# Kernel optimization log

Hardware: AMD Instinct MI355X
Metric: run time of the kernel (lower is better)

Reference implementation:

```python
import jax, jax.numpy as jnp
import numpy as np

B, S, H, I = 4, 2048, 4096, 11008

def setup_inputs() -> dict:
    key = jax.random.key(0)
    k0, k1, k2, k3 = jax.random.split(key, 4)
    scale = 0.02  # typical init scale for stability
    return {
        "x": jax.random.normal(k0, (B, S, H), dtype=jnp.float32),
        "w_gate": jax.random.normal(k1, (I, H), dtype=jnp.float32) * scale,
        "w_up": jax.random.normal(k2, (I, H), dtype=jnp.float32) * scale,
        "w_down": jax.random.normal(k3, (H, I), dtype=jnp.float32) * scale,
    }

def reference(x, w_gate, w_up, w_down):
    # gate = x @ w_gate^T, up = x @ w_up^T  (torch F.linear convention)
    gate = jnp.einsum("bsh,ih->bsi", x, w_gate)
    up = jnp.einsum("bsh,ih->bsi", x, w_up)
    inter = jax.nn.silu(gate) * up  # SwiGLU
    return jnp.einsum("bsi,hi->bsh", inter, w_down)
```

## Files before the change

kernel.cpp:

```cpp
#include <hip/hip_runtime.h>
#include <hip/hip_bf16.h>
#include <stdint.h>

static constexpr int Hd = 4096;
static constexpr int Id = 11008;
static constexpr int Md = 8192;

using short8 = __attribute__((ext_vector_type(8))) short;
using f32x4  = __attribute__((ext_vector_type(4))) float;

__device__ __forceinline__ unsigned short f2bf(float x) {
    union { float f; unsigned u; } v; v.f = x;
    unsigned r = v.u + 0x7FFF + ((v.u >> 16) & 1);
    return (unsigned short)(r >> 16);
}

typedef const __attribute__((address_space(1))) unsigned int* as1_u32p;
typedef __attribute__((address_space(3))) unsigned int* as3_u32p;

__device__ __forceinline__ void gload16(const unsigned short* g, unsigned short* l) {
    __builtin_amdgcn_global_load_lds((as1_u32p)(const void*)g, (as3_u32p)(void*)l, 16, 0, 0);
}

#define AOFF(r, c) ((((r) * 8) + ((c) ^ ((r) & 7))) * 8)

#define LGKM0() do { asm volatile("s_waitcnt lgkmcnt(0)" ::: "memory"); \
                     __builtin_amdgcn_sched_barrier(0); } while (0)
#define LGKMC8() do { asm volatile("s_waitcnt lgkmcnt(8)" ::: "memory"); } while (0)
#define VMCNT(n) do { asm volatile("s_waitcnt vmcnt(" #n ")" ::: "memory"); \
                      __builtin_amdgcn_sched_barrier(0); } while (0)
#define BARRIER() do { asm volatile("" ::: "memory"); __builtin_amdgcn_s_barrier(); \
                       asm volatile("" ::: "memory"); } while (0)

__global__ __launch_bounds__(256) void k_cvt4(
    const float* __restrict__ s0, unsigned short* __restrict__ d0, int n0,
    const float* __restrict__ s1, unsigned short* __restrict__ d1, int n1,
    const float* __restrict__ s2, unsigned short* __restrict__ d2, int n2,
    const float* __restrict__ s3, unsigned short* __restrict__ d3, int n3)
{
    const int total = n0 + n1 + n2 + n3;
    int i = blockIdx.x * blockDim.x + threadIdx.x;
    const int stride = gridDim.x * blockDim.x;
    for (; i < total; i += stride) {
        const float* s; unsigned short* d; int j = i;
        if (j < n0) { s = s0; d = d0; }
        else { j -= n0;
            if (j < n1) { s = s1; d = d1; }
            else { j -= n1;
                if (j < n2) { s = s2; d = d2; }
                else { j -= n2; s = s3; d = d3; }
            }
        }
        f32x4 a = *(const f32x4*)(s + (size_t)j * 8);
        f32x4 b = *(const f32x4*)(s + (size_t)j * 8 + 4);
        short8 v;
        v[0] = (short)f2bf(a[0]); v[1] = (short)f2bf(a[1]);
        v[2] = (short)f2bf(a[2]); v[3] = (short)f2bf(a[3]);
        v[4] = (short)f2bf(b[0]); v[5] = (short)f2bf(b[1]);
        v[6] = (short)f2bf(b[2]); v[7] = (short)f2bf(b[3]);
        *reinterpret_cast<short8*>(d + (size_t)j * 8) = v;
    }
}

template<int D>
__device__ __forceinline__ void ug_body(
    unsigned short (&As)[2][2][8192], unsigned short (&Gs)[2][8192], unsigned short (&Us)[2][8192],
    const unsigned short* pA0, const unsigned short* pA1,
    const unsigned short* pG0, const unsigned short* pG1,
    const unsigned short* pU0, const unsigned short* pU1,
    int stoff, bool pf,
    int wm, int wn, int r16, int kg, int wave,
    f32x4 (&accg)[8][2], f32x4 (&accu)[8][2])
{
    constexpr size_t hK = (size_t)128 * Hd;
    short8 af[4][2], gf[2][2], uf[2][2];

    #pragma unroll
    for (int mi = 0; mi < 4; ++mi)
        #pragma unroll
        for (int kk = 0; kk < 2; ++kk)
            af[mi][kk] = *(const short8*)&As[D][wm][AOFF(mi * 16 + r16, kk * 4 + kg)];
    #pragma unroll
    for (int ni = 0; ni < 2; ++ni)
        #pragma unroll
        for (int kk = 0; kk < 2; ++kk)
            gf[ni][kk] = *(const short8*)&Gs[D][AOFF(wn * 32 + ni * 16 + r16, kk * 4 + kg)];
    LGKMC8();
    BARRIER();
    LGKM0();
    __builtin_amdgcn_s_setprio(1);
    #pragma unroll
    for (int mi = 0; mi < 4; ++mi)
        #pragma unroll
        for (int ni = 0; ni < 2; ++ni)
            #pragma unroll
            for (int kk = 0; kk < 2; ++kk)
                accg[mi][ni] = __builtin_amdgcn_mfma_f32_16x16x32_bf16(af[mi][kk], gf[ni][kk], accg[mi][ni], 0, 0, 0);
    __builtin_amdgcn_s_setprio(0);
    BARRIER();

    if (pf) {
        gload16(pG0 + stoff, &Gs[D][wave * 512]);
        gload16(pG1 + stoff, &Gs[D][4096 + wave * 512]);
    }
    #pragma unroll
    for (int ni = 0; ni < 2; ++ni)
        #pragma unroll
        for (int kk = 0; kk < 2; ++kk)
            uf[ni][kk] = *(const short8*)&Us[D][AOFF(wn * 32 + ni * 16 + r16, kk * 4 + kg)];
    BARRIER();
    LGKM0();
    __builtin_amdgcn_s_setprio(1);
    #pragma unroll
    for (int mi = 0; mi < 4; ++mi)
        #pragma unroll
        for (int ni = 0; ni < 2; ++ni)
            #pragma unroll
            for (int kk = 0; kk < 2; ++kk)
                accu[mi][ni] = __builtin_amdgcn_mfma_f32_16x16x32_bf16(af[mi][kk], uf[ni][kk], accu[mi][ni], 0, 0, 0);
    __builtin_amdgcn_s_setprio(0);
    BARRIER();

    if (pf) {
        gload16(pU0 + stoff, &Us[D][wave * 512]);
        gload16(pU1 + stoff, &Us[D][4096 + wave * 512]);
    }
    #pragma unroll
    for (int mi = 0; mi < 4; ++mi)
        #pragma unroll
        for (int kk = 0; kk < 2; ++kk)
            af[mi][kk] = *(const short8*)&As[D][wm][AOFF((mi + 4) * 16 + r16, kk * 4 + kg)];
    BARRIER();
    LGKM0();
    __builtin_amdgcn_s_setprio(1);
    #pragma unroll
    for (int mi = 0; mi < 4; ++mi)
        #pragma unroll
        for (int ni = 0; ni < 2; ++ni)
            #pragma unroll
            for (int kk = 0; kk < 2; ++kk)
                accg[mi + 4][ni] = __builtin_amdgcn_mfma_f32_16x16x32_bf16(af[mi][kk], gf[ni][kk], accg[mi + 4][ni], 0, 0, 0);
    __builtin_amdgcn_s_setprio(0);
    BARRIER();

    if (pf) {
        gload16(pA0 + stoff,      &As[D][0][wave * 512]);
        gload16(pA1 + stoff,      &As[D][0][4096 + wave * 512]);
        gload16(pA0 + hK + stoff, &As[D][1][wave * 512]);
        gload16(pA1 + hK + stoff, &As[D][1][4096 + wave * 512]);
    }
    __builtin_amdgcn_s_setprio(1);
    #pragma unroll
    for (int mi = 0; mi < 4; ++mi)
        #pragma unroll
        for (int ni = 0; ni < 2; ++ni)
            #pragma unroll
            for (int kk = 0; kk < 2; ++kk)
                accu[mi + 4][ni] = __builtin_amdgcn_mfma_f32_16x16x32_bf16(af[mi][kk], uf[ni][kk], accu[mi + 4][ni], 0, 0, 0);
    __builtin_amdgcn_s_setprio(0);
    if (pf) { VMCNT(8); }
    else    { VMCNT(0); }
    BARRIER();
}

__global__ __launch_bounds__(512, 2) void k_upgate(
    const unsigned short* __restrict__ A,
    const unsigned short* __restrict__ G,
    const unsigned short* __restrict__ U,
    unsigned short* __restrict__ inter)
{
    __shared__ unsigned short As[2][2][8192];
    __shared__ unsigned short Gs[2][8192];
    __shared__ unsigned short Us[2][8192];

    const int tid  = threadIdx.x;
    const int wave = tid >> 6;
    const int lane = tid & 63;
    const int wm   = wave >> 2;
    const int wn   = wave & 3;
    const int r16  = lane & 15;
    const int kg   = lane >> 4;

    const int nwg = gridDim.x;
    const int bid = blockIdx.x;
    const int swz = (bid & 7) * (nwg >> 3) + (bid >> 3);
    const int grp = swz / 688;
    const int rem = swz % 688;
    const int m0  = (grp * 8 + (rem & 7)) * 256;
    const int n0  = (rem >> 3) * 128;

    const int i0 = tid,       r0 = i0 >> 3;
    const int i1 = 512 + tid, r1 = i1 >> 3;
    const int cc0 = (i0 & 7) ^ (r0 & 7);
    const int cc1 = (i1 & 7) ^ (r1 & 7);
    constexpr size_t hK = (size_t)128 * Hd;

    const unsigned short* pA0 = A + (size_t)(m0 + r0) * Hd + cc0 * 8;
    const unsigned short* pA1 = A + (size_t)(m0 + r1) * Hd + cc1 * 8;
    const unsigned short* pG0 = G + (size_t)(n0 + r0) * Hd + cc0 * 8;
    const unsigned short* pG1 = G + (size_t)(n0 + r1) * Hd + cc1 * 8;
    const unsigned short* pU0 = U + (size_t)(n0 + r0) * Hd + cc0 * 8;
    const unsigned short* pU1 = U + (size_t)(n0 + r1) * Hd + cc1 * 8;

    f32x4 accg[8][2] = {};
    f32x4 accu[8][2] = {};

    constexpr int NT = Hd >> 6;

    gload16(pA0,      &As[0][0][wave * 512]);
    gload16(pA1,      &As[0][0][4096 + wave * 512]);
    gload16(pA0 + hK, &As[0][1][wave * 512]);
    gload16(pA1 + hK, &As[0][1][4096 + wave * 512]);
    gload16(pG0,      &Gs[0][wave * 512]);
    gload16(pG1,      &Gs[0][4096 + wave * 512]);
    gload16(pU0,      &Us[0][wave * 512]);
    gload16(pU1,      &Us[0][4096 + wave * 512]);
    gload16(pA0 + 64,      &As[1][0][wave * 512]);
    gload16(pA1 + 64,      &As[1][0][4096 + wave * 512]);
    gload16(pA0 + hK + 64, &As[1][1][wave * 512]);
    gload16(pA1 + hK + 64, &As[1][1][4096 + wave * 512]);
    gload16(pG0 + 64,      &Gs[1][wave * 512]);
    gload16(pG1 + 64,      &Gs[1][4096 + wave * 512]);
    gload16(pU0 + 64,      &Us[1][wave * 512]);
    gload16(pU1 + 64,      &Us[1][4096 + wave * 512]);
    VMCNT(8);
    BARRIER();

    for (int kt = 0; kt < NT; kt += 2) {
        const bool pf0 = (kt + 2) < NT;
        const bool pf1 = (kt + 3) < NT;
        ug_body<0>(As, Gs, Us, pA0, pA1, pG0, pG1, pU0, pU1, 128, pf0,
                   wm, wn, r16, kg, wave, accg, accu);
        ug_body<1>(As, Gs, Us, pA0, pA1, pG0, pG1, pU0, pU1, 192, pf1,
                   wm, wn, r16, kg, wave, accg, accu);
        pA0 += 128; pA1 += 128; pG0 += 128; pG1 += 128; pU0 += 128; pU1 += 128;
    }

    #pragma unroll
    for (int mi = 0; mi < 8; ++mi)
        #pragma unroll
        for (int ni = 0; ni < 2; ++ni) {
            const int row = m0 + wm * 128 + mi * 16 + kg * 4;
            const int col = n0 + wn * 32 + ni * 16 + r16;
            f32x4 g = accg[mi][ni], u = accu[mi][ni];
            #pragma unroll
            for (int rr = 0; rr < 4; ++rr) {
                float gv = g[rr];
                float s  = gv / (1.0f + __expf(-gv));
                inter[(size_t)(row + rr) * Id + col] = f2bf(s * u[rr]);
            }
        }
}

template<int D>
__device__ __forceinline__ void ktile_body(
    unsigned short (&As)[2][2][8192], unsigned short (&Bs)[2][2][8192],
    const unsigned short* pA0, const unsigned short* pA1,
    const unsigned short* pB0, const unsigned short* pB1,
    size_t hK, int stoff, bool pf,
    int wm, int wn, int r16, int kg, int wave,
    f32x4 (&acc)[8][4], short8 (&af)[4][2], short8 (&b0f)[2][2], short8 (&b1f)[2][2])
{
    #pragma unroll
    for (int mi = 0; mi < 4; ++mi)
        #pragma unroll
        for (int kk = 0; kk < 2; ++kk)
            af[mi][kk] = *(const short8*)&As[D][wm][AOFF(mi * 16 + r16, kk * 4 + kg)];
    #pragma unroll
    for (int ni = 0; ni < 2; ++ni)
        #pragma unroll
        for (int kk = 0; kk < 2; ++kk)
            b0f[ni][kk] = *(const short8*)&Bs[D][wn >> 1][AOFF((wn & 1) * 64 + ni * 16 + r16, kk * 4 + kg)];
    LGKMC8();
    BARRIER();
    LGKM0();
    __builtin_amdgcn_s_setprio(1);
    #pragma unroll
    for (int mi = 0; mi < 4; ++mi)
        #pragma unroll
        for (int ni = 0; ni < 2; ++ni)
            #pragma unroll
            for (int kk = 0; kk < 2; ++kk)
                acc[mi][ni] = __builtin_amdgcn_mfma_f32_16x16x32_bf16(af[mi][kk], b0f[ni][kk], acc[mi][ni], 0, 0, 0);
    __builtin_amdgcn_s_setprio(0);
    BARRIER();

    #pragma unroll
    for (int ni = 0; ni < 2; ++ni)
        #pragma unroll
        for (int kk = 0; kk < 2; ++kk)
            b1f[ni][kk] = *(const short8*)&Bs[D][wn >> 1][AOFF((wn & 1) * 64 + (ni + 2) * 16 + r16, kk * 4 + kg)];
    BARRIER();
    LGKM0();
    __builtin_amdgcn_s_setprio(1);
    #pragma unroll
    for (int mi = 0; mi < 4; ++mi)
        #pragma unroll
        for (int ni = 0; ni < 2; ++ni)
            #pragma unroll
            for (int kk = 0; kk < 2; ++kk)
                acc[mi][ni + 2] = __builtin_amdgcn_mfma_f32_16x16x32_bf16(af[mi][kk], b1f[ni][kk], acc[mi][ni + 2], 0, 0, 0);
    __builtin_amdgcn_s_setprio(0);
    BARRIER();

    if (pf) {
        gload16(pB0 + stoff,      &Bs[D][0][wave * 512]);
        gload16(pB1 + stoff,      &Bs[D][0][4096 + wave * 512]);
        gload16(pB0 + hK + stoff, &Bs[D][1][wave * 512]);
        gload16(pB1 + hK + stoff, &Bs[D][1][4096 + wave * 512]);
    }
    #pragma unroll
    for (int mi = 0; mi < 4; ++mi)
        #pragma unroll
        for (int kk = 0; kk < 2; ++kk)
            af[mi][kk] = *(const short8*)&As[D][wm][AOFF((mi + 4) * 16 + r16, kk * 4 + kg)];
    BARRIER();
    LGKM0();
    __builtin_amdgcn_s_setprio(1);
    #pragma unroll
    for (int mi = 0; mi < 4; ++mi)
        #pragma unroll
        for (int ni = 0; ni < 2; ++ni)
            #pragma unroll
            for (int kk = 0; kk < 2; ++kk)
                acc[mi + 4][ni + 2] = __builtin_amdgcn_mfma_f32_16x16x32_bf16(af[mi][kk], b1f[ni][kk], acc[mi + 4][ni + 2], 0, 0, 0);
    __builtin_amdgcn_s_setprio(0);
    BARRIER();

    if (pf) {
        gload16(pA0 + stoff,      &As[D][0][wave * 512]);
        gload16(pA1 + stoff,      &As[D][0][4096 + wave * 512]);
        gload16(pA0 + hK + stoff, &As[D][1][wave * 512]);
        gload16(pA1 + hK + stoff, &As[D][1][4096 + wave * 512]);
    }
    __builtin_amdgcn_s_setprio(1);
    #pragma unroll
    for (int mi = 0; mi < 4; ++mi)
        #pragma unroll
        for (int ni = 0; ni < 2; ++ni)
            #pragma unroll
            for (int kk = 0; kk < 2; ++kk)
                acc[mi + 4][ni] = __builtin_amdgcn_mfma_f32_16x16x32_bf16(af[mi][kk], b0f[ni][kk], acc[mi + 4][ni], 0, 0, 0);
    __builtin_amdgcn_s_setprio(0);
    if (pf) { VMCNT(8); }
    else    { VMCNT(0); }
    BARRIER();
}

__global__ __launch_bounds__(512, 2) void k_down(
    const unsigned short* __restrict__ A, const unsigned short* __restrict__ B,
    float* __restrict__ Cf, const int K, const int ldC)
{
    __shared__ unsigned short As[2][2][8192];
    __shared__ unsigned short Bs[2][2][8192];

    const int tid  = threadIdx.x;
    const int wave = tid >> 6;
    const int lane = tid & 63;
    const int wm   = wave >> 2;
    const int wn   = wave & 3;
    const int r16  = lane & 15;
    const int kg   = lane >> 4;

    const int nwg = gridDim.x;
    const int bid = blockIdx.x;
    const int swz = (bid & 7) * (nwg >> 3) + (bid >> 3);
    const int grp = swz / 128;
    const int rem = swz % 128;
    const int m0  = (grp * 8 + (rem & 7)) * 256;
    const int n0  = (rem >> 3) * 256;

    const int i0 = tid,       r0 = i0 >> 3;
    const int i1 = 512 + tid, r1 = i1 >> 3;
    const int cc0 = (i0 & 7) ^ (r0 & 7);
    const int cc1 = (i1 & 7) ^ (r1 & 7);
    const size_t hK = (size_t)128 * K;

    const unsigned short* pA0 = A + (size_t)(m0 + r0) * K + cc0 * 8;
    const unsigned short* pA1 = A + (size_t)(m0 + r1) * K + cc1 * 8;
    const unsigned short* pB0 = B + (size_t)(n0 + r0) * K + cc0 * 8;
    const unsigned short* pB1 = B + (size_t)(n0 + r1) * K + cc1 * 8;

    f32x4 acc[8][4] = {};
    short8 af[4][2], b0f[2][2], b1f[2][2];

    const int NT = K >> 6;

    gload16(pA0,      &As[0][0][wave * 512]);
    gload16(pA1,      &As[0][0][4096 + wave * 512]);
    gload16(pA0 + hK, &As[0][1][wave * 512]);
    gload16(pA1 + hK, &As[0][1][4096 + wave * 512]);
    gload16(pB0,      &Bs[0][0][wave * 512]);
    gload16(pB1,      &Bs[0][0][4096 + wave * 512]);
    gload16(pB0 + hK, &Bs[0][1][wave * 512]);
    gload16(pB1 + hK, &Bs[0][1][4096 + wave * 512]);
    gload16(pA0 + 64,      &As[1][0][wave * 512]);
    gload16(pA1 + 64,      &As[1][0][4096 + wave * 512]);
    gload16(pA0 + hK + 64, &As[1][1][wave * 512]);
    gload16(pA1 + hK + 64, &As[1][1][4096 + wave * 512]);
    gload16(pB0 + 64,      &Bs[1][0][wave * 512]);
    gload16(pB1 + 64,      &Bs[1][0][4096 + wave * 512]);
    gload16(pB0 + hK + 64, &Bs[1][1][wave * 512]);
    gload16(pB1 + hK + 64, &Bs[1][1][4096 + wave * 512]);
    VMCNT(8);
    BARRIER();

    for (int kt = 0; kt < NT; kt += 2) {
        const bool pf0 = (kt + 2) < NT;
        const bool pf1 = (kt + 3) < NT;
        ktile_body<0>(As, Bs, pA0, pA1, pB0, pB1, hK, 128, pf0,
                      wm, wn, r16, kg, wave, acc, af, b0f, b1f);
        ktile_body<1>(As, Bs, pA0, pA1, pB0, pB1, hK, 192, pf1,
                      wm, wn, r16, kg, wave, acc, af, b0f, b1f);
        pA0 += 128; pA1 += 128; pB0 += 128; pB1 += 128;
    }

    #pragma unroll
    for (int mi = 0; mi < 8; ++mi)
        #pragma unroll
        for (int ni = 0; ni < 4; ++ni) {
            const int row = m0 + wm * 128 + mi * 16 + kg * 4;
            const int col = n0 + wn * 64 + ni * 16 + r16;
            f32x4 v = acc[mi][ni];
            #pragma unroll
            for (int rr = 0; rr < 4; ++rr)
                Cf[(size_t)(row + rr) * ldC + col] = v[rr];
        }
}

extern "C" void kernel_launch(void* const* d_in, const int* in_sizes, int n_in,
                              void* d_out, int out_size, void* d_ws, size_t ws_size,
                              hipStream_t stream) {
    const float* x  = (const float*)d_in[0];
    const float* wg = (const float*)d_in[1];
    const float* wu = (const float*)d_in[2];
    const float* wd = (const float*)d_in[3];
    float* out = (float*)d_out;

    unsigned short* inter = (unsigned short*)d_ws;
    unsigned short* xb  = (unsigned short*)((char*)d_ws + (size_t)Md * Id * 2);
    unsigned short* wgb = xb  + (size_t)Md * Hd;
    unsigned short* wub = wgb + (size_t)Id * Hd;
    unsigned short* wdb = wub + (size_t)Id * Hd;

    k_cvt4<<<dim3(2048), dim3(256), 0, stream>>>(
        x,  xb,  Md * Hd / 8,
        wg, wgb, Id * Hd / 8,
        wu, wub, Id * Hd / 8,
        wd, wdb, Id * Hd / 8);

    k_upgate<<<dim3((Md / 256) * (Id / 128)), dim3(512), 0, stream>>>(xb, wgb, wub, inter);
    k_down<<<dim3((Md / 256) * (Hd / 256)), dim3(512), 0, stream>>>(inter, wdb, out, Id, Hd);
}
```

Baseline: 2.068 ms.

## Restagger prefetch so A tiles load one step ahead into alternate buffer

The prefetch schedule in both GEMM kernels changes so the A tile for the next k-step is loaded into the other LDS buffer early in the current step, while B (or gate/up) tiles stay two steps ahead in the same buffer. The prologue no longer preloads the second A stage, and the wait counts drop to 4 outstanding loads. The intent is to spread global loads more evenly across the MFMA phases and shorten the startup. The cost is a shorter lookahead for A, so its latency is less hidden, and a more fragile buffer-reuse pattern that depends on the barriers being placed correctly.

Measured after the change: 2.338 ms. 1.13x slower.

```diff
diff --git a/kernel.cpp b/kernel.cpp
--- a/kernel.cpp
+++ b/kernel.cpp
@@ -68,13 +68,17 @@
     const unsigned short* pA0, const unsigned short* pA1,
     const unsigned short* pG0, const unsigned short* pG1,
     const unsigned short* pU0, const unsigned short* pU1,
-    int stoff, bool pf,
+    int stA, int stGU, bool pfA, bool pfGU,
     int wm, int wn, int r16, int kg, int wave,
     f32x4 (&accg)[8][2], f32x4 (&accu)[8][2])
 {
     constexpr size_t hK = (size_t)128 * Hd;
     short8 af[4][2], gf[2][2], uf[2][2];
 
+    if (pfA) {
+        gload16(pA0 + stA, &As[D ^ 1][0][wave * 512]);
+        gload16(pA1 + stA, &As[D ^ 1][0][4096 + wave * 512]);
+    }
     #pragma unroll
     for (int mi = 0; mi < 4; ++mi)
         #pragma unroll
@@ -99,9 +103,9 @@
     __builtin_amdgcn_s_setprio(0);
     BARRIER();
 
-    if (pf) {
-        gload16(pG0 + stoff, &Gs[D][wave * 512]);
-        gload16(pG1 + stoff, &Gs[D][4096 + wave * 512]);
+    if (pfA) {
+        gload16(pA0 + hK + stA, &As[D ^ 1][1][wave * 512]);
+        gload16(pA1 + hK + stA, &As[D ^ 1][1][4096 + wave * 512]);
     }
     #pragma unroll
     for (int ni = 0; ni < 2; ++ni)
@@ -121,9 +125,9 @@
     __builtin_amdgcn_s_setprio(0);
     BARRIER();
 
-    if (pf) {
-        gload16(pU0 + stoff, &Us[D][wave * 512]);
-        gload16(pU1 + stoff, &Us[D][4096 + wave * 512]);
+    if (pfGU) {
+        gload16(pG0 + stGU, &Gs[D][wave * 512]);
+        gload16(pG1 + stGU, &Gs[D][4096 + wave * 512]);
     }
     #pragma unroll
     for (int mi = 0; mi < 4; ++mi)
@@ -143,11 +147,9 @@
     __builtin_amdgcn_s_setprio(0);
     BARRIER();
 
-    if (pf) {
-        gload16(pA0 + stoff,      &As[D][0][wave * 512]);
-        gload16(pA1 + stoff,      &As[D][0][4096 + wave * 512]);
-        gload16(pA0 + hK + stoff, &As[D][1][wave * 512]);
-        gload16(pA1 + hK + stoff, &As[D][1][4096 + wave * 512]);
+    if (pfGU) {
+        gload16(pU0 + stGU, &Us[D][wave * 512]);
+        gload16(pU1 + stGU, &Us[D][4096 + wave * 512]);
     }
     __builtin_amdgcn_s_setprio(1);
     #pragma unroll
@@ -158,8 +160,8 @@
             for (int kk = 0; kk < 2; ++kk)
                 accu[mi + 4][ni] = __builtin_amdgcn_mfma_f32_16x16x32_bf16(af[mi][kk], uf[ni][kk], accu[mi + 4][ni], 0, 0, 0);
     __builtin_amdgcn_s_setprio(0);
-    if (pf) { VMCNT(8); }
-    else    { VMCNT(0); }
+    if (pfGU) { VMCNT(4); }
+    else      { VMCNT(0); }
     BARRIER();
 }
 
@@ -215,24 +217,18 @@
     gload16(pG1,      &Gs[0][4096 + wave * 512]);
     gload16(pU0,      &Us[0][wave * 512]);
     gload16(pU1,      &Us[0][4096 + wave * 512]);
-    gload16(pA0 + 64,      &As[1][0][wave * 512]);
-    gload16(pA1 + 64,      &As[1][0][4096 + wave * 512]);
-    gload16(pA0 + hK + 64, &As[1][1][wave * 512]);
-    gload16(pA1 + hK + 64, &As[1][1][4096 + wave * 512]);
-    gload16(pG0 + 64,      &Gs[1][wave * 512]);
-    gload16(pG1 + 64,      &Gs[1][4096 + wave * 512]);
-    gload16(pU0 + 64,      &Us[1][wave * 512]);
-    gload16(pU1 + 64,      &Us[1][4096 + wave * 512]);
-    VMCNT(8);
+    gload16(pG0 + 64, &Gs[1][wave * 512]);
+    gload16(pG1 + 64, &Gs[1][4096 + wave * 512]);
+    gload16(pU0 + 64, &Us[1][wave * 512]);
+    gload16(pU1 + 64, &Us[1][4096 + wave * 512]);
+    VMCNT(4);
     BARRIER();
 
     for (int kt = 0; kt < NT; kt += 2) {
-        const bool pf0 = (kt + 2) < NT;
-        const bool pf1 = (kt + 3) < NT;
-        ug_body<0>(As, Gs, Us, pA0, pA1, pG0, pG1, pU0, pU1, 128, pf0,
-                   wm, wn, r16, kg, wave, accg, accu);
-        ug_body<1>(As, Gs, Us, pA0, pA1, pG0, pG1, pU0, pU1, 192, pf1,
-                   wm, wn, r16, kg, wave, accg, accu);
+        ug_body<0>(As, Gs, Us, pA0, pA1, pG0, pG1, pU0, pU1,
+                   64, 128, true, (kt + 2) < NT, wm, wn, r16, kg, wave, accg, accu);
+        ug_body<1>(As, Gs, Us, pA0, pA1, pG0, pG1, pU0, pU1,
+                   128, 192, (kt + 2) < NT, (kt + 3) < NT, wm, wn, r16, kg, wave, accg, accu);
         pA0 += 128; pA1 += 128; pG0 += 128; pG1 += 128; pU0 += 128; pU1 += 128;
     }
 
@@ -257,10 +253,14 @@
     unsigned short (&As)[2][2][8192], unsigned short (&Bs)[2][2][8192],
     const unsigned short* pA0, const unsigned short* pA1,
     const unsigned short* pB0, const unsigned short* pB1,
-    size_t hK, int stoff, bool pf,
+    size_t hK, int stA, int stB, bool pfA, bool pfB,
     int wm, int wn, int r16, int kg, int wave,
     f32x4 (&acc)[8][4], short8 (&af)[4][2], short8 (&b0f)[2][2], short8 (&b1f)[2][2])
 {
+    if (pfA) {
+        gload16(pA0 + stA, &As[D ^ 1][0][wave * 512]);
+        gload16(pA1 + stA, &As[D ^ 1][0][4096 + wave * 512]);
+    }
     #pragma unroll
     for (int mi = 0; mi < 4; ++mi)
         #pragma unroll
@@ -285,6 +285,10 @@
     __builtin_amdgcn_s_setprio(0);
     BARRIER();
 
+    if (pfA) {
+        gload16(pA0 + hK + stA, &As[D ^ 1][1][wave * 512]);
+        gload16(pA1 + hK + stA, &As[D ^ 1][1][4096 + wave * 512]);
+    }
     #pragma unroll
     for (int ni = 0; ni < 2; ++ni)
         #pragma unroll
@@ -303,11 +307,9 @@
     __builtin_amdgcn_s_setprio(0);
     BARRIER();
 
-    if (pf) {
-        gload16(pB0 + stoff,      &Bs[D][0][wave * 512]);
-        gload16(pB1 + stoff,      &Bs[D][0][4096 + wave * 512]);
-        gload16(pB0 + hK + stoff, &Bs[D][1][wave * 512]);
-        gload16(pB1 + hK + stoff, &Bs[D][1][4096 + wave * 512]);
+    if (pfB) {
+        gload16(pB0 + stB, &Bs[D][0][wave * 512]);
+        gload16(pB1 + stB, &Bs[D][0][4096 + wave * 512]);
     }
     #pragma unroll
     for (int mi = 0; mi < 4; ++mi)
@@ -327,11 +329,9 @@
     __builtin_amdgcn_s_setprio(0);
     BARRIER();
 
-    if (pf) {
-        gload16(pA0 + stoff,      &As[D][0][wave * 512]);
-        gload16(pA1 + stoff,      &As[D][0][4096 + wave * 512]);
-        gload16(pA0 + hK + stoff, &As[D][1][wave * 512]);
-        gload16(pA1 + hK + stoff, &As[D][1][4096 + wave * 512]);
+    if (pfB) {
+        gload16(pB0 + hK + stB, &Bs[D][1][wave * 512]);
+        gload16(pB1 + hK + stB, &Bs[D][1][4096 + wave * 512]);
     }
     __builtin_amdgcn_s_setprio(1);
     #pragma unroll
@@ -342,8 +342,8 @@
             for (int kk = 0; kk < 2; ++kk)
                 acc[mi + 4][ni] = __builtin_amdgcn_mfma_f32_16x16x32_bf16(af[mi][kk], b0f[ni][kk], acc[mi + 4][ni], 0, 0, 0);
     __builtin_amdgcn_s_setprio(0);
-    if (pf) { VMCNT(8); }
-    else    { VMCNT(0); }
+    if (pfB) { VMCNT(4); }
+    else     { VMCNT(0); }
     BARRIER();
 }
 
@@ -394,24 +394,18 @@
     gload16(pB1,      &Bs[0][0][4096 + wave * 512]);
     gload16(pB0 + hK, &Bs[0][1][wave * 512]);
     gload16(pB1 + hK, &Bs[0][1][4096 + wave * 512]);
-    gload16(pA0 + 64,      &As[1][0][wave * 512]);
-    gload16(pA1 + 64,      &As[1][0][4096 + wave * 512]);
-    gload16(pA0 + hK + 64, &As[1][1][wave * 512]);
-    gload16(pA1 + hK + 64, &As[1][1][4096 + wave * 512]);
     gload16(pB0 + 64,      &Bs[1][0][wave * 512]);
     gload16(pB1 + 64,      &Bs[1][0][4096 + wave * 512]);
     gload16(pB0 + hK + 64, &Bs[1][1][wave * 512]);
     gload16(pB1 + hK + 64, &Bs[1][1][4096 + wave * 512]);
-    VMCNT(8);
+    VMCNT(4);
     BARRIER();
 
     for (int kt = 0; kt < NT; kt += 2) {
-        const bool pf0 = (kt + 2) < NT;
-        const bool pf1 = (kt + 3) < NT;
-        ktile_body<0>(As, Bs, pA0, pA1, pB0, pB1, hK, 128, pf0,
-                      wm, wn, r16, kg, wave, acc, af, b0f, b1f);
-        ktile_body<1>(As, Bs, pA0, pA1, pB0, pB1, hK, 192, pf1,
-                      wm, wn, r16, kg, wave, acc, af, b0f, b1f);
+        ktile_body<0>(As, Bs, pA0, pA1, pB0, pB1, hK, 64, 128,
+                      true, (kt + 2) < NT, wm, wn, r16, kg, wave, acc, af, b0f, b1f);
+        ktile_body<1>(As, Bs, pA0, pA1, pB0, pB1, hK, 128, 192,
+                      (kt + 2) < NT, (kt + 3) < NT, wm, wn, r16, kg, wave, acc, af, b0f, b1f);
         pA0 += 128; pA1 += 128; pB0 += 128; pB1 += 128;
     }
 
```
